# Kernel tuning notes

Hardware: AMD Instinct MI355X
Metric: run time of the kernel (lower is better)

## Reference

```python
import jax, jax.numpy as jnp
import numpy as np

LN_EPS = 1e-5

def _ln(x, g, b):
    m = x.mean(-1, keepdims=True)
    v = x.var(-1, keepdims=True)
    return (x - m) * jax.lax.rsqrt(v + LN_EPS) * g + b

def _sru_layer(x, W, vc, bias, g, be):
    # x: (L, B, d); W: (d, k*h) with k=3 (d==h) or k=4 (d!=h)
    L, B, _ = x.shape
    h = vc.shape[0] // 2
    xn = _ln(x, g, be)
    k = W.shape[1] // h
    U = (xn @ W).reshape(L, B, k, h)
    u0, u1, u2 = U[:, :, 0], U[:, :, 1], U[:, :, 2]
    res = U[:, :, 3] if k == 4 else xn
    vf, vr = vc[:h], vc[h:]
    bf, br = bias[:h], bias[h:]
    def step(c, inp):
        a0, a1, a2, rt = inp
        f = jax.nn.sigmoid(a1 + vf * c + bf)
        r = jax.nn.sigmoid(a2 + vr * c + br)
        c2 = f * c + (1.0 - f) * a0
        return c2, r * c2 + (1.0 - r) * rt
    _, hs = jax.lax.scan(step, jnp.zeros((B, h), x.dtype), (u0, u1, u2, res))
    return hs  # (L, B, h)

def _lstm(x, Wih, Whh, bih, bhh):
    # x: (L, B, d); PyTorch gate order i, f, g, o
    L, B, _ = x.shape
    H = Whh.shape[1]
    pre = x @ Wih.T + (bih + bhh)  # (L, B, 4H)
    def step(carry, p):
        hp, cp = carry
        gates = p + hp @ Whh.T
        i, f, g, o = jnp.split(gates, 4, axis=-1)
        c = jax.nn.sigmoid(f) * cp + jax.nn.sigmoid(i) * jnp.tanh(g)
        hn = jax.nn.sigmoid(o) * jnp.tanh(c)
        return (hn, c), hn
    z = jnp.zeros((B, H), x.dtype)
    _, hs = jax.lax.scan(step, (z, z), pre)
    return hs

def setup_inputs() -> dict:
    key = jax.random.key(0)
    ks = jax.random.split(key, 12)
    B, T, F, H, LS, V = 16, 1024, 128, 1024, 1024, 1000
    s = 0.05
    inp = {}
    inp['x'] = jax.random.normal(ks[0], (B, T, F), dtype=jnp.float32)
    # first SRU layer (input F != H -> k=4)
    inp['w0'] = jax.random.normal(ks[1], (F, 4 * H), dtype=jnp.float32) * s
    inp['vc0'] = jax.random.normal(ks[2], (2 * H,), dtype=jnp.float32) * s
    inp['b0'] = jnp.zeros((2 * H,), jnp.float32)
    inp['g0'] = jnp.ones((F,), jnp.float32)
    inp['be0'] = jnp.zeros((F,), jnp.float32)
    # 6 stacked SRU layers with d==h (3 remaining first_layer + 3 sru_layers)
    inp['Ws'] = jax.random.normal(ks[3], (6, H, 3 * H), dtype=jnp.float32) * s
    inp['VCs'] = jax.random.normal(ks[4], (6, 2 * H), dtype=jnp.float32) * s
    inp['Bs'] = jnp.zeros((6, 2 * H), jnp.float32)
    inp['Gs'] = jnp.ones((6, H), jnp.float32)
    inp['Bes'] = jnp.zeros((6, H), jnp.float32)
    # LSTM
    inp['Wih'] = jax.random.normal(ks[5], (4 * LS, H), dtype=jnp.float32) * s
    inp['Whh'] = jax.random.normal(ks[6], (4 * LS, LS), dtype=jnp.float32) * s
    inp['bih'] = jnp.zeros((4 * LS,), jnp.float32)
    inp['bhh'] = jnp.zeros((4 * LS,), jnp.float32)
    # classifier: LayerNorm + Linear(no bias) to V+1
    inp['gh'] = jnp.ones((LS,), jnp.float32)
    inp['bh'] = jnp.zeros((LS,), jnp.float32)
    inp['Wout'] = jax.random.normal(ks[7], (LS, V + 1), dtype=jnp.float32) * s
    return inp

def reference(x, w0, vc0, b0, g0, be0, Ws, VCs, Bs, Gs, Bes,
              Wih, Whh, bih, bhh, gh, bh, Wout):
    t = jnp.transpose(x, (1, 0, 2))  # (T, B, F)
    t = _sru_layer(t, w0, vc0, b0, g0, be0)
    for i in range(3):
        t = _sru_layer(t, Ws[i], VCs[i], Bs[i], Gs[i], Bes[i])
    # AvgPool1d(kernel=2, stride=2) over time
    L = t.shape[0]
    t = t[: (L // 2) * 2].reshape(L // 2, 2, t.shape[1], t.shape[2]).mean(axis=1)
    for i in range(3, 6):
        t = _sru_layer(t, Ws[i], VCs[i], Bs[i], Gs[i], Bes[i])
    t = _lstm(t, Wih, Whh, bih, bhh)
    t = jnp.transpose(t, (1, 0, 2))  # (B, T/2, lstm_dim)
    return _ln(t, gh, bh) @ Wout  # (B, T/2, n_vocab+1)
```

## Files before the change

kernel.cpp:

```cpp
#include <hip/hip_runtime.h>

typedef __bf16 bf16x8 __attribute__((ext_vector_type(8)));
typedef float f32x4 __attribute__((ext_vector_type(4)));

__device__ __forceinline__ unsigned short f2bf(float f) {
  unsigned u = __builtin_bit_cast(unsigned, f);
  u += 0x7fffu + ((u >> 16) & 1u);
  return (unsigned short)(u >> 16);
}
__device__ __forceinline__ float bf2f(unsigned short h) {
  unsigned u = ((unsigned)h) << 16;
  return __builtin_bit_cast(float, u);
}
__device__ __forceinline__ float sigmoidf_(float x) {
  return 1.f / (1.f + __expf(-x));
}
__device__ __forceinline__ float tanhf_(float x) {
  return 1.f - 2.f / (__expf(2.f * x) + 1.f);
}
__device__ __forceinline__ void gload16(const unsigned short* g, unsigned short* l) {
  __builtin_amdgcn_global_load_lds((const __attribute__((address_space(1))) void*)g,
                                   (__attribute__((address_space(3))) void*)l, 16, 0, 0);
}


__global__ __launch_bounds__(256) void k_castf(const float* __restrict__ src,
                                               unsigned short* __restrict__ dst, int n4) {
  int i = blockIdx.x * 256 + threadIdx.x;
  if (i < n4) {
    float4 v = ((const float4*)src)[i];
    ushort4 o;
    o.x = f2bf(v.x); o.y = f2bf(v.y); o.z = f2bf(v.z); o.w = f2bf(v.w);
    ((ushort4*)dst)[i] = o;
  }
}

__global__ void k_cast_t(const float* __restrict__ src, unsigned short* __restrict__ dst,
                         int K, int N) {
  __shared__ float tile[32][33];
  int nx = blockIdx.x * 32, ky = blockIdx.y * 32;
  int tx = threadIdx.x, ty = threadIdx.y;
  #pragma unroll
  for (int j = 0; j < 32; j += 8) {
    int n = nx + tx, k = ky + ty + j;
    tile[ty + j][tx] = (n < N) ? src[(long)k * N + n] : 0.f;
  }
  __syncthreads();
  #pragma unroll
  for (int j = 0; j < 32; j += 8) {
    int n = nx + ty + j, k = ky + tx;
    dst[(long)n * K + k] = f2bf(tile[tx][ty + j]);
  }
}


__global__ __launch_bounds__(128) void k_ln0(const float* __restrict__ x,
                                             unsigned short* __restrict__ out,
                                             const float* __restrict__ g,
                                             const float* __restrict__ be) {
  int row = blockIdx.x;
  int t = row >> 4, b = row & 15;
  const float* src = x + ((long)b * 1024 + t) * 128;
  int i = threadIdx.x;
  float v = src[i];
  float s = v, q = v * v;
  #pragma unroll
  for (int off = 32; off > 0; off >>= 1) {
    s += __shfl_down(s, off);
    q += __shfl_down(q, off);
  }
  __shared__ float red[4];
  int wv = i >> 6;
  if ((i & 63) == 0) { red[wv] = s; red[2 + wv] = q; }
  __syncthreads();
  float S = red[0] + red[1], Q = red[2] + red[3];
  float mean = S * (1.f / 128.f);
  float var = Q * (1.f / 128.f) - mean * mean;
  float rs = rsqrtf(var + 1e-5f);
  out[(long)row * 128 + i] = f2bf((v - mean) * rs * g[i] + be[i]);
}

__global__ __launch_bounds__(256) void k_ln(const float* __restrict__ in,
                                            unsigned short* __restrict__ out16,
                                            const float* __restrict__ g,
                                            const float* __restrict__ be, int avg) {
  int row = blockIdx.x;
  int tid = threadIdx.x;
  int col = tid * 4;
  float xv[4];
  if (avg) {
    int l = row >> 4, b = row & 15;
    const float* r0 = in + ((long)(2 * l) * 16 + b) * 1024;
    const float* r1 = r0 + 16 * 1024;
    float4 a = *(const float4*)(r0 + col);
    float4 bb = *(const float4*)(r1 + col);
    xv[0] = 0.5f * (a.x + bb.x);
    xv[1] = 0.5f * (a.y + bb.y);
    xv[2] = 0.5f * (a.z + bb.z);
    xv[3] = 0.5f * (a.w + bb.w);
  } else {
    float4 a = *(const float4*)(in + (long)row * 1024 + col);
    xv[0] = a.x; xv[1] = a.y; xv[2] = a.z; xv[3] = a.w;
  }
  float s = xv[0] + xv[1] + xv[2] + xv[3];
  float q = xv[0]*xv[0] + xv[1]*xv[1] + xv[2]*xv[2] + xv[3]*xv[3];
  #pragma unroll
  for (int off = 32; off > 0; off >>= 1) {
    s += __shfl_down(s, off);
    q += __shfl_down(q, off);
  }
  __shared__ float red[8];
  int wv = tid >> 6;
  if ((tid & 63) == 0) { red[wv] = s; red[4 + wv] = q; }
  __syncthreads();
  float S = red[0] + red[1] + red[2] + red[3];
  float Q = red[4] + red[5] + red[6] + red[7];
  float mean = S * (1.f / 1024.f);
  float var = Q * (1.f / 1024.f) - mean * mean;
  float rs = rsqrtf(var + 1e-5f);
  ushort4 o;
  o.x = f2bf((xv[0] - mean) * rs * g[col + 0] + be[col + 0]);
  o.y = f2bf((xv[1] - mean) * rs * g[col + 1] + be[col + 1]);
  o.z = f2bf((xv[2] - mean) * rs * g[col + 2] + be[col + 2]);
  o.w = f2bf((xv[3] - mean) * rs * g[col + 3] + be[col + 3]);
  *(ushort4*)(out16 + (long)row * 1024 + col) = o;
}

template <int MODE>
__global__ __launch_bounds__(256) void k_gemm(const unsigned short* __restrict__ A,
                                              const unsigned short* __restrict__ Bt,
                                              void* __restrict__ Cout,
                                              const float* __restrict__ bias1,
                                              const float* __restrict__ bias2,
                                              int M, int N, int K) {
  __shared__ unsigned short As[128][64];
  __shared__ unsigned short Bs[128][64];
  const int bn = blockIdx.x * 128, bm = blockIdx.y * 128;
  const int tid = threadIdx.x;
  const int wave = tid >> 6, lane = tid & 63;
  const int wm = (wave >> 1) * 64, wn = (wave & 1) * 64;
  const int l15 = lane & 15, kq = lane >> 4;
  f32x4 acc[4][4] = {};
  const int r0 = tid >> 3;
  const int c0 = (tid & 7) * 8;
  const unsigned short* Ap = A + (long)(bm + r0) * K + c0;
  const unsigned short* Bp = Bt + (long)(bn + r0) * K + c0;
  for (int kb = 0; kb < K; kb += 64) {
    #pragma unroll
    for (int i = 0; i < 4; i++) {
      gload16(Ap + (long)(i * 32) * K + kb, &As[i * 32 + r0][c0]);
      gload16(Bp + (long)(i * 32) * K + kb, &Bs[i * 32 + r0][c0]);
    }
    __syncthreads();
    #pragma unroll
    for (int kk = 0; kk < 2; kk++) {
      const int kcol = kk * 32 + kq * 8;
      bf16x8 a[4], b[4];
      #pragma unroll
      for (int m = 0; m < 4; m++) a[m] = *(const bf16x8*)&As[wm + m * 16 + l15][kcol];
      #pragma unroll
      for (int n = 0; n < 4; n++) b[n] = *(const bf16x8*)&Bs[wn + n * 16 + l15][kcol];
      #pragma unroll
      for (int m = 0; m < 4; m++)
        #pragma unroll
        for (int n = 0; n < 4; n++)
          acc[m][n] = __builtin_amdgcn_mfma_f32_16x16x32_bf16(a[m], b[n], acc[m][n], 0, 0, 0);
    }
    __syncthreads();
  }
  #pragma unroll
  for (int m = 0; m < 4; m++)
    #pragma unroll
    for (int n = 0; n < 4; n++) {
      #pragma unroll
      for (int r = 0; r < 4; r++) {
        int gm = bm + wm + m * 16 + kq * 4 + r;
        int gn = bn + wn + n * 16 + l15;
        float v = acc[m][n][r];
        if (MODE == 0) {
          ((float*)Cout)[(long)gm * N + gn] = v;
        } else if (MODE == 1) {
          v += bias1[gn] + bias2[gn];
          ((float*)Cout)[(long)gm * N + gn] = v;
        } else {
          if (gn < 1001) {
            long oi = ((long)(gm & 15) * 512 + (gm >> 4)) * 1001 + gn;
            ((float*)Cout)[oi] = v;
          }
        }
      }
    }
}

__global__ __launch_bounds__(64) void k_scan(const float* __restrict__ U,
                                             const unsigned short* __restrict__ Res16,
                                             const float* __restrict__ vc,
                                             const float* __restrict__ bias,
                                             float* __restrict__ Hout,
                                             unsigned short* __restrict__ H16,
                                             float* __restrict__ cbuf,
                                             int Lc, int k4, int first) {
  int tid = blockIdx.x * 64 + threadIdx.x;
  int b = tid >> 10, hc = tid & 1023;
  float vf = vc[hc], vr = vc[1024 + hc];
  float bfv = bias[hc], brv = bias[1024 + hc];
  const int k = k4 ? 4 : 3;
  const long strideT = 16L * k * 1024;
  const long base0 = (long)b * k * 1024 + hc;
  const long rbase = (long)b * 1024 + hc;
  const long rstride = 16 * 1024;
  float c = first ? 0.f : cbuf[tid];
  for (int t0 = 0; t0 < Lc; t0 += 8) {
    float u0[8], u1[8], u2[8], rr[8];
    #pragma unroll
    for (int j = 0; j < 8; j++) {
      long o = base0 + (long)(t0 + j) * strideT;
      u0[j] = U[o];
      u1[j] = U[o + 1024];
      u2[j] = U[o + 2048];
      rr[j] = k4 ? U[o + 3072] : bf2f(Res16[rbase + (long)(t0 + j) * rstride]);
    }
    #pragma unroll
    for (int j = 0; j < 8; j++) {
      float f = sigmoidf_(u1[j] + vf * c + bfv);
      float r = sigmoidf_(u2[j] + vr * c + brv);
      c = f * c + (1.f - f) * u0[j];
      float h = r * c + (1.f - r) * rr[j];
      long oo = rbase + (long)(t0 + j) * rstride;
      Hout[oo] = h;
      if (H16) H16[oo] = f2bf(h);
    }
  }
  cbuf[tid] = c;
}

__global__ __launch_bounds__(256) void k_lstm_step(
    const unsigned short* __restrict__ Whhb,
    const float* __restrict__ Prep,
    const unsigned short* __restrict__ hin,
    unsigned short* __restrict__ hout,
    float* __restrict__ cst,
    float* __restrict__ HsOutp) {
  const int tid = threadIdx.x;
  const int wave = tid >> 6, lane = tid & 63;
  const int j = blockIdx.x;
  const int c0 = j * 4;
  const int l15 = lane & 15, kq = lane >> 4;
  const int wrow = (l15 >> 2) * 1024 + c0 + (l15 & 3);
  f32x4 acc = {0.f, 0.f, 0.f, 0.f};
  const unsigned short* hp = hin + l15 * 1024 + wave * 256 + kq * 8;
  const unsigned short* wp = Whhb + (long)wrow * 1024 + wave * 256 + kq * 8;
  #pragma unroll
  for (int kb = 0; kb < 256; kb += 32) {
    bf16x8 a = *(const bf16x8*)(hp + kb);
    bf16x8 w = *(const bf16x8*)(wp + kb);
    acc = __builtin_amdgcn_mfma_f32_16x16x32_bf16(a, w, acc, 0, 0, 0);
  }
  __shared__ float P[4][16][16];
  __shared__ float G[16][16];
  #pragma unroll
  for (int r = 0; r < 4; r++) {
    int m = kq * 4 + r;
    P[wave][m][l15] = acc[r];
  }
  __syncthreads();
  {
    int m = tid >> 4, col = tid & 15;
    int gate = col >> 2, ch = c0 + (col & 3);
    float pre = Prep[(long)m * 4096 + gate * 1024 + ch];
    G[m][col] = P[0][m][col] + P[1][m][col] + P[2][m][col] + P[3][m][col] + pre;
  }
  __syncthreads();
  if (tid < 64) {
    int m = tid & 15, chl = tid >> 4;
    float ig = G[m][0 * 4 + chl];
    float fg = G[m][1 * 4 + chl];
    float gg = G[m][2 * 4 + chl];
    float og = G[m][3 * 4 + chl];
    long ci = (long)m * 1024 + c0 + chl;
    float cold = cst[ci];
    float cn = sigmoidf_(fg) * cold + sigmoidf_(ig) * tanhf_(gg);
    float hn = sigmoidf_(og) * tanhf_(cn);
    cst[ci] = cn;
    hout[ci] = f2bf(hn);
    HsOutp[(long)m * 1024 + c0 + chl] = hn;
  }
}


extern "C" void kernel_launch(void* const* d_in, const int* in_sizes, int n_in,
                              void* d_out, int out_size, void* d_ws, size_t ws_size,
                              hipStream_t stream) {
  const float* x    = (const float*)d_in[0];
  const float* w0   = (const float*)d_in[1];
  const float* vc0  = (const float*)d_in[2];
  const float* b0   = (const float*)d_in[3];
  const float* g0   = (const float*)d_in[4];
  const float* be0  = (const float*)d_in[5];
  const float* Ws   = (const float*)d_in[6];
  const float* VCs  = (const float*)d_in[7];
  const float* Bsi  = (const float*)d_in[8];
  const float* Gs   = (const float*)d_in[9];
  const float* Bes  = (const float*)d_in[10];
  const float* Wih  = (const float*)d_in[11];
  const float* Whh  = (const float*)d_in[12];
  const float* bih  = (const float*)d_in[13];
  const float* bhh  = (const float*)d_in[14];
  const float* gh   = (const float*)d_in[15];
  const float* bh   = (const float*)d_in[16];
  const float* Wout = (const float*)d_in[17];

  char* ws = (char*)d_ws;
  size_t off = 0;
  auto alloc = [&](size_t bytes) {
    size_t r = off;
    off += (bytes + 255) & ~(size_t)255;
    return r;
  };
  unsigned short* W0t   = (unsigned short*)(ws + alloc(4096UL * 128 * 2));
  unsigned short* Wst   = (unsigned short*)(ws + alloc(6UL * 3072 * 1024 * 2));
  unsigned short* Wihb  = (unsigned short*)(ws + alloc(4096UL * 1024 * 2));
  unsigned short* Whhb  = (unsigned short*)(ws + alloc(4096UL * 1024 * 2));
  unsigned short* Woutt = (unsigned short*)(ws + alloc(1024UL * 1024 * 2));
  unsigned short* Xn    = (unsigned short*)(ws + alloc(16384UL * 1024 * 2));
  float*          Hbuf  = (float*)(ws + alloc(16384UL * 1024 * 4));
  float*          Ubuf  = (float*)(ws + alloc(4096UL * 4096 * 4));
  unsigned short* hb0   = (unsigned short*)(ws + alloc(16UL * 1024 * 2));
  unsigned short* hb1   = (unsigned short*)(ws + alloc(16UL * 1024 * 2));
  float*          cst   = (float*)(ws + alloc(16UL * 1024 * 4));
  float*          cscan = (float*)(ws + alloc(16UL * 1024 * 4));
  float*          HsOut = Hbuf;
  unsigned short* H16l6 = Xn + 8192L * 1024;
  unsigned short* LNout = Xn;

  k_cast_t<<<dim3(4096 / 32, 128 / 32), dim3(32, 8), 0, stream>>>(w0, W0t, 128, 4096);
  for (int i = 0; i < 6; i++)
    k_cast_t<<<dim3(3072 / 32, 1024 / 32), dim3(32, 8), 0, stream>>>(
        Ws + (long)i * 1024 * 3072, Wst + (long)i * 3072 * 1024, 1024, 3072);
  k_cast_t<<<dim3(1024 / 32, 1024 / 32), dim3(32, 8), 0, stream>>>(Wout, Woutt, 1024, 1001);
  k_castf<<<4096, 256, 0, stream>>>(Wih, Wihb, 4096 * 1024 / 4);
  k_castf<<<4096, 256, 0, stream>>>(Whh, Whhb, 4096 * 1024 / 4);
  hipMemsetAsync(hb0, 0, 32768 + 32768 + 65536, stream);

  const int CH_T = 256;
  const int CH_R = CH_T * 16;

  k_ln0<<<16384, 128, 0, stream>>>(x, Xn, g0, be0);
  for (int c = 0; c < 4; c++) {
    k_gemm<0><<<dim3(4096 / 128, CH_R / 128), 256, 0, stream>>>(
        Xn + (long)c * CH_R * 128, W0t, Ubuf, nullptr, nullptr, CH_R, 4096, 128);
    k_scan<<<256, 64, 0, stream>>>(Ubuf, nullptr, vc0, b0,
                                   Hbuf + (long)c * CH_R * 1024, nullptr, cscan,
                                   CH_T, 1, c == 0);
  }

  for (int i = 0; i < 6; i++) {
    int L = (i < 3) ? 1024 : 512;
    int rows = L * 16;
    int avg = (i == 3) ? 1 : 0;
    k_ln<<<rows, 256, 0, stream>>>(Hbuf, Xn, Gs + i * 1024, Bes + i * 1024, avg);
    int nch = rows / CH_R;
    for (int c = 0; c < nch; c++) {
      k_gemm<0><<<dim3(3072 / 128, CH_R / 128), 256, 0, stream>>>(
          Xn + (long)c * CH_R * 1024, Wst + (long)i * 3072 * 1024, Ubuf, nullptr, nullptr,
          CH_R, 3072, 1024);
      k_scan<<<256, 64, 0, stream>>>(Ubuf, Xn + (long)c * CH_R * 1024,
                                     VCs + i * 2048, Bsi + i * 2048,
                                     Hbuf + (long)c * CH_R * 1024,
                                     (i == 5) ? (H16l6 + (long)c * CH_R * 1024) : nullptr,
                                     cscan, CH_T, 0, c == 0);
    }
  }

  const int LCH_T = 128, LCH_R = LCH_T * 16;
  for (int c = 0; c < 4; c++) {
    k_gemm<1><<<dim3(4096 / 128, LCH_R / 128), 256, 0, stream>>>(
        H16l6 + (long)c * LCH_R * 1024, Wihb, Ubuf, bih, bhh, LCH_R, 4096, 1024);
    for (int tl = 0; tl < LCH_T; tl++) {
      int tg = c * LCH_T + tl;
      unsigned short* hin = (tg & 1) ? hb1 : hb0;
      unsigned short* hout = (tg & 1) ? hb0 : hb1;
      k_lstm_step<<<256, 256, 0, stream>>>(Whhb, Ubuf + (long)tl * 16 * 4096, hin, hout,
                                           cst, HsOut + (long)tg * 16 * 1024);
    }
  }

  k_ln<<<8192, 256, 0, stream>>>(HsOut, LNout, gh, bh, 0);
  k_gemm<2><<<dim3(1024 / 128, 8192 / 128), 256, 0, stream>>>(LNout, Woutt, d_out, nullptr,
                                                              nullptr, 8192, 1024, 1024);
}
```

Before: 6.257 ms.

## Replace per-step LSTM launches with persistent kernel and grid flag barrier

```diff
diff --git a/kernel.cpp b/kernel.cpp
--- a/kernel.cpp
+++ b/kernel.cpp
@@ -234,57 +234,84 @@
   cbuf[tid] = c;
 }
 
-__global__ __launch_bounds__(256) void k_lstm_step(
-    const unsigned short* __restrict__ Whhb,
-    const float* __restrict__ Prep,
-    const unsigned short* __restrict__ hin,
-    unsigned short* __restrict__ hout,
+__global__ __launch_bounds__(1024) void k_lstm_seq(
+    const unsigned short* __restrict__ Whh,
+    const float* __restrict__ U,
+    unsigned short* __restrict__ hb0,
+    unsigned short* __restrict__ hb1,
     float* __restrict__ cst,
-    float* __restrict__ HsOutp) {
+    float* __restrict__ HsOut,
+    unsigned* __restrict__ flags,
+    int nT, int tg0) {
+  __shared__ unsigned short wlds[65536];
+  __shared__ float P[4][16][66];
+  __shared__ float G[16][68];
   const int tid = threadIdx.x;
+  const int j = blockIdx.x;
+  const int c0 = j * 16;
+
+  #pragma unroll
+  for (int i = 0; i < 8; i++) {
+    int m = tid + i * 1024;
+    int g = m >> 11, ks = (m >> 6) & 31, kq2 = (m >> 4) & 3, l = m & 15;
+    bf16x8 v = *(const bf16x8*)(Whh + (long)(g * 1024 + c0 + l) * 1024 + ks * 32 + kq2 * 8);
+    *(bf16x8*)&wlds[m * 8] = v;
+  }
+  float creg = 0.f;
+  if (tid < 256) creg = cst[(long)(tid >> 4) * 1024 + c0 + (tid & 15)];
+  __syncthreads();
+
   const int wave = tid >> 6, lane = tid & 63;
-  const int j = blockIdx.x;
-  const int c0 = j * 4;
+  const int g = wave & 3, kgrp = wave >> 2;
   const int l15 = lane & 15, kq = lane >> 4;
-  const int wrow = (l15 >> 2) * 1024 + c0 + (l15 & 3);
-  f32x4 acc = {0.f, 0.f, 0.f, 0.f};
-  const unsigned short* hp = hin + l15 * 1024 + wave * 256 + kq * 8;
-  const unsigned short* wp = Whhb + (long)wrow * 1024 + wave * 256 + kq * 8;
-  #pragma unroll
-  for (int kb = 0; kb < 256; kb += 32) {
-    bf16x8 a = *(const bf16x8*)(hp + kb);
-    bf16x8 w = *(const bf16x8*)(wp + kb);
-    acc = __builtin_amdgcn_mfma_f32_16x16x32_bf16(a, w, acc, 0, 0, 0);
-  }
-  __shared__ float P[4][16][16];
-  __shared__ float G[16][16];
-  #pragma unroll
-  for (int r = 0; r < 4; r++) {
-    int m = kq * 4 + r;
-    P[wave][m][l15] = acc[r];
-  }
-  __syncthreads();
-  {
-    int m = tid >> 4, col = tid & 15;
-    int gate = col >> 2, ch = c0 + (col & 3);
-    float pre = Prep[(long)m * 4096 + gate * 1024 + ch];
-    G[m][col] = P[0][m][col] + P[1][m][col] + P[2][m][col] + P[3][m][col] + pre;
-  }
-  __syncthreads();
-  if (tid < 64) {
-    int m = tid & 15, chl = tid >> 4;
-    float ig = G[m][0 * 4 + chl];
-    float fg = G[m][1 * 4 + chl];
-    float gg = G[m][2 * 4 + chl];
-    float og = G[m][3 * 4 + chl];
-    long ci = (long)m * 1024 + c0 + chl;
-    float cold = cst[ci];
-    float cn = sigmoidf_(fg) * cold + sigmoidf_(ig) * tanhf_(gg);
-    float hn = sigmoidf_(og) * tanhf_(cn);
-    cst[ci] = cn;
-    hout[ci] = f2bf(hn);
-    HsOutp[(long)m * 1024 + c0 + chl] = hn;
-  }
+  const unsigned short* wfrag = &wlds[((g * 32 + kgrp * 8) * 64 + lane) * 8];
+
+  for (int t = 0; t < nT; t++) {
+    const int tg = tg0 + t;
+    const unsigned short* hin = (tg & 1) ? hb1 : hb0;
+    unsigned short* hout = (tg & 1) ? hb0 : hb1;
+    f32x4 acc = {0.f, 0.f, 0.f, 0.f};
+    const unsigned short* hp = hin + l15 * 1024 + kgrp * 256 + kq * 8;
+    #pragma unroll
+    for (int s = 0; s < 8; s++) {
+      bf16x8 a = *(const bf16x8*)(hp + s * 32);
+      bf16x8 b = *(const bf16x8*)(wfrag + (long)s * 64 * 8);
+      acc = __builtin_amdgcn_mfma_f32_16x16x32_bf16(a, b, acc, 0, 0, 0);
+    }
+    #pragma unroll
+    for (int r = 0; r < 4; r++) P[kgrp][kq * 4 + r][g * 16 + l15] = acc[r];
+    __syncthreads();
+    {
+      int m = tid >> 6, gc = tid & 63;
+      int gg = gc >> 4, cc = gc & 15;
+      float pre = U[((long)t * 16 + m) * 4096 + gg * 1024 + c0 + cc];
+      G[m][gc] = P[0][m][gc] + P[1][m][gc] + P[2][m][gc] + P[3][m][gc] + pre;
+    }
+    __syncthreads();
+    if (tid < 256) {
+      int m = tid >> 4, cc = tid & 15;
+      float ig = G[m][cc], fg = G[m][16 + cc], gg2 = G[m][32 + cc], og = G[m][48 + cc];
+      float cn = sigmoidf_(fg) * creg + sigmoidf_(ig) * tanhf_(gg2);
+      float hn = sigmoidf_(og) * tanhf_(cn);
+      creg = cn;
+      hout[m * 1024 + c0 + cc] = f2bf(hn);
+      HsOut[((long)tg * 16 + m) * 1024 + c0 + cc] = hn;
+    }
+    __syncthreads();
+    const unsigned gen = (unsigned)(tg + 1);
+    if (tid == 0)
+      __hip_atomic_store(&flags[j], gen, __ATOMIC_RELEASE, __HIP_MEMORY_SCOPE_AGENT);
+    if (tid < 64) {
+      unsigned v;
+      do {
+        __builtin_amdgcn_s_sleep(1);
+        v = __hip_atomic_load(&flags[tid], __ATOMIC_RELAXED, __HIP_MEMORY_SCOPE_AGENT);
+      } while (!__all(v >= gen));
+      __builtin_amdgcn_fence(__ATOMIC_ACQUIRE, "agent");
+    }
+    __syncthreads();
+  }
+  if (tid < 256) cst[(long)(tid >> 4) * 1024 + c0 + (tid & 15)] = creg;
 }
 
 
@@ -329,6 +356,7 @@
   unsigned short* hb1   = (unsigned short*)(ws + alloc(16UL * 1024 * 2));
   float*          cst   = (float*)(ws + alloc(16UL * 1024 * 4));
   float*          cscan = (float*)(ws + alloc(16UL * 1024 * 4));
+  unsigned*       flags = (unsigned*)(ws + alloc(64UL * 4));
   float*          HsOut = Hbuf;
   unsigned short* H16l6 = Xn + 8192L * 1024;
   unsigned short* LNout = Xn;
@@ -340,7 +368,7 @@
   k_cast_t<<<dim3(1024 / 32, 1024 / 32), dim3(32, 8), 0, stream>>>(Wout, Woutt, 1024, 1001);
   k_castf<<<4096, 256, 0, stream>>>(Wih, Wihb, 4096 * 1024 / 4);
   k_castf<<<4096, 256, 0, stream>>>(Whh, Whhb, 4096 * 1024 / 4);
-  hipMemsetAsync(hb0, 0, 32768 + 32768 + 65536, stream);
+  hipMemsetAsync(hb0, 0, 32768 + 32768 + 65536 + 65536 + 256, stream);
 
   const int CH_T = 256;
   const int CH_R = CH_T * 16;
@@ -376,13 +404,8 @@
   for (int c = 0; c < 4; c++) {
     k_gemm<1><<<dim3(4096 / 128, LCH_R / 128), 256, 0, stream>>>(
         H16l6 + (long)c * LCH_R * 1024, Wihb, Ubuf, bih, bhh, LCH_R, 4096, 1024);
-    for (int tl = 0; tl < LCH_T; tl++) {
-      int tg = c * LCH_T + tl;
-      unsigned short* hin = (tg & 1) ? hb1 : hb0;
-      unsigned short* hout = (tg & 1) ? hb0 : hb1;
-      k_lstm_step<<<256, 256, 0, stream>>>(Whhb, Ubuf + (long)tl * 16 * 4096, hin, hout,
-                                           cst, HsOut + (long)tg * 16 * 1024);
-    }
+    k_lstm_seq<<<64, 1024, 0, stream>>>(Whhb, Ubuf, hb0, hb1, cst, HsOut, flags,
+                                        LCH_T, c * LCH_T);
   }
 
   k_ln<<<8192, 256, 0, stream>>>(HsOut, LNout, gh, bh, 0);
```

After: 8.009 ms. +28.0%, slower.
